# Performance work log

Hardware: AMD Instinct MI355X
Metric: run time of the kernel (lower is better)

The kernel has to match this reference:

```python
import jax, jax.numpy as jnp
import numpy as np

B, C, H, W, K = 64, 64, 32, 32, 512  # batch, embedding_dim, latent HxW, num_embeddings
COMMITMENT_COST = 0.25


def setup_inputs() -> dict:
    key = jax.random.key(0)
    k1, k2 = jax.random.split(key)
    inputs = jax.random.normal(k1, (B, C, H, W), dtype=jnp.float32)
    # nn.Embedding weight initialized uniform(-1/K, 1/K)
    weight = jax.random.uniform(k2, (K, C), minval=-1.0 / K, maxval=1.0 / K, dtype=jnp.float32)
    return {"inputs": inputs, "weight": weight}


def reference(inputs, weight):
    # NCHW -> NHWC
    x = jnp.transpose(inputs, (0, 2, 3, 1))  # [B,H,W,C]
    b, h, w, c = x.shape
    flat = x.reshape(-1, c)  # [N, C], N = B*H*W

    distances = (jnp.sum(flat * flat, axis=1, keepdims=True)
                 + jnp.sum(weight * weight, axis=1)[None, :]
                 - 2.0 * flat @ weight.T)

    idx = jnp.argmin(distances, axis=1)  # [N]
    encodings = jax.nn.one_hot(idx, weight.shape[0], dtype=flat.dtype)  # [N, K]

    # gather codebook vectors (same math as encodings @ weight)
    quantized = weight[idx].reshape(x.shape)  # [B,H,W,C]

    e_latent = jnp.mean((jax.lax.stop_gradient(quantized) - x) ** 2, axis=(1, 2, 3))
    q_latent = jnp.mean((quantized - jax.lax.stop_gradient(x)) ** 2, axis=(1, 2, 3))
    loss = q_latent + COMMITMENT_COST * e_latent  # [B]

    # straight-through estimator
    quantized_st = x + jax.lax.stop_gradient(quantized - x)

    avg_probs = jnp.mean(encodings, axis=0)  # [K]
    perplexity = jnp.exp(-jnp.sum(avg_probs * jnp.log(avg_probs + 1e-10)))

    q_out = jnp.transpose(quantized_st, (0, 3, 1, 2))  # back to NCHW
    enc_idx = idx.reshape(b, -1)  # [B, H*W]
    return (q_out, loss, perplexity, encodings, enc_idx, distances)
```

## Files before the change

### kernel.cpp

```cpp
#include <hip/hip_runtime.h>
#include <stdint.h>
#include <math.h>

#pragma clang fp contract(off)

#define B_   64
#define C_   64
#define HW_  1024
#define K_   512
#define N_   65536

#define OUT_Q    0ull
#define OUT_LOSS 4194304ull
#define OUT_PERP 4194368ull
#define OUT_ENC  4194369ull
#define OUT_IDX  37748801ull
#define OUT_DIST 37814337ull

#define WS_WT     0ull
#define WS_WNORM  131072ull
#define WS_HIST   133120ull
#define WS_SUMSQ  135168ull
#define WS_ZERO_BYTES (512*4 + 64*4)

typedef float f32x4 __attribute__((ext_vector_type(4)));

static __device__ __forceinline__ void nt_store4(float* p, float a, float b,
                                                 float c, float d) {
  f32x4 v = {a, b, c, d};
  __builtin_nontemporal_store(v, (f32x4*)p);
}

__global__ __launch_bounds__(256) void vq_prep(const float* __restrict__ w,
                                               float* __restrict__ wt,
                                               float* __restrict__ wnorm) {
  const int t = threadIdx.x;
  const int g = blockIdx.x * 256 + t;
  const int c = g >> 9;
  const int k = g & 511;
  wt[g] = w[k * 64 + c];

  if (blockIdx.x < 16) {
    const int row = g >> 3;
    const int j = g & 7;
    float s = 0.f;
    for (int i = 0; i < 8; ++i) {
      float v = w[row * 64 + 8 * i + j];
      float sq = v * v;
      s = s + sq;
    }
    float o1 = __shfl_xor(s, 1); s = s + o1;
    float o2 = __shfl_xor(s, 2); s = s + o2;
    float o4 = __shfl_xor(s, 4); s = s + o4;
    if (j == 0) wnorm[row] = s;
  }
}

__global__ __launch_bounds__(256, 4) void vq_main(const float* __restrict__ x,
                                                  const float* __restrict__ wt,
                                                  const float* __restrict__ wnorm,
                                                  float* __restrict__ out,
                                                  int* __restrict__ hist,
                                                  float* __restrict__ sumsq) {
  __shared__ float x_s[64 * 32];
  __shared__ float an_s[32];
  __shared__ int   kmin_s[32];
  __shared__ float red_s[4];

  const int t   = threadIdx.x;
  const int blk = blockIdx.x;
  const int n0  = blk * 32;
  const int b   = n0 >> 10;
  const int hw0 = n0 & 1023;
  const int wid = t >> 6;
  const int l   = t & 63;

  {
    const float* xb = x + (size_t)b * 65536 + hw0;
    const int c0 = t >> 3;
    const int m4 = (t & 7) * 4;
#pragma unroll
    for (int i = 0; i < 2; ++i) {
      int c = i * 32 + c0;
      float4 v = *(const float4*)(xb + (size_t)c * 1024 + m4);
      *(float4*)(&x_s[c * 32 + m4]) = v;
    }
  }
  __syncthreads();

  {
    const int r = t >> 3, j = t & 7;
    float s = 0.f;
#pragma unroll
    for (int i = 0; i < 8; ++i) {
      float v = x_s[(8 * i + j) * 32 + r];
      float sq = v * v;
      s = s + sq;
    }
    float o1 = __shfl_xor(s, 1); s = s + o1;
    float o2 = __shfl_xor(s, 2); s = s + o2;
    float o4 = __shfl_xor(s, 4); s = s + o4;
    if (j == 0) an_s[r] = s;
  }

  float wn[8];
  *(float4*)(wn)     = *(const float4*)(wnorm + 4 * l);
  *(float4*)(wn + 4) = *(const float4*)(wnorm + 256 + 4 * l);

  float acc[8][8];
#pragma unroll
  for (int i = 0; i < 8; ++i)
#pragma unroll
    for (int j = 0; j < 8; ++j) acc[i][j] = 0.f;

  const float* const wl = wt + 4 * l;
  const float* const xw = x_s + 8 * wid;
  float4 w0 = *(const float4*)(wl);
  float4 w1 = *(const float4*)(wl + 256);
#pragma unroll 2
  for (int c = 0; c < 64; ++c) {
    const int cn = (c + 1) & 63;
    const float4 nw0 = *(const float4*)(wl + cn * 512);
    const float4 nw1 = *(const float4*)(wl + cn * 512 + 256);
    float xv[8];
    *(float4*)(xv)     = *(const float4*)(xw + c * 32);
    *(float4*)(xv + 4) = *(const float4*)(xw + c * 32 + 4);
    const float wv0[4] = {w0.x, w0.y, w0.z, w0.w};
    const float wv1[4] = {w1.x, w1.y, w1.z, w1.w};
#pragma unroll
    for (int i = 0; i < 8; ++i) {
#pragma unroll
      for (int j = 0; j < 4; ++j) {
        acc[i][j]     = __builtin_fmaf(xv[i], wv0[j], acc[i][j]);
        acc[i][j + 4] = __builtin_fmaf(xv[i], wv1[j], acc[i][j + 4]);
      }
    }
    w0 = nw0; w1 = nw1;
  }

  const int m_base = 8 * wid;
  float vb[8]; int kb[8];
#pragma unroll
  for (int i = 0; i < 8; ++i) {
    const float an = an_s[m_base + i];
#pragma unroll
    for (int j = 0; j < 8; ++j) {
      float tt = an + wn[j];
      acc[i][j] = __builtin_fmaf(-2.f, acc[i][j], tt);
    }
    float v = acc[i][0]; int k = 4 * l;
#pragma unroll
    for (int j = 1; j < 8; ++j) {
      const int kj = ((j >> 2) << 8) + 4 * l + (j & 3);
      if (acc[i][j] < v) { v = acc[i][j]; k = kj; }
    }
    vb[i] = v; kb[i] = k;
  }

#pragma unroll
  for (int d = 1; d < 64; d <<= 1) {
#pragma unroll
    for (int i = 0; i < 8; ++i) {
      float v2 = __shfl_xor(vb[i], d);
      int   k2 = __shfl_xor(kb[i], d);
      if (v2 < vb[i] || (v2 == vb[i] && k2 < kb[i])) { vb[i] = v2; kb[i] = k2; }
    }
  }

  float* const dist_o = out + OUT_DIST;
  float* const enc_o  = out + OUT_ENC;
#pragma unroll
  for (int i = 0; i < 8; ++i) {
    const int m = m_base + i;
    const size_t n = (size_t)(n0 + m);
    float* dr = dist_o + n * 512;
    float* er = enc_o  + n * 512;
    nt_store4(dr + 4 * l,       acc[i][0], acc[i][1], acc[i][2], acc[i][3]);
    nt_store4(dr + 256 + 4 * l, acc[i][4], acc[i][5], acc[i][6], acc[i][7]);
    const int kbi = kb[i];
    const int k0 = 4 * l;
    nt_store4(er + 4 * l,
              (k0 + 0 == kbi) ? 1.f : 0.f, (k0 + 1 == kbi) ? 1.f : 0.f,
              (k0 + 2 == kbi) ? 1.f : 0.f, (k0 + 3 == kbi) ? 1.f : 0.f);
    nt_store4(er + 256 + 4 * l,
              (k0 + 256 == kbi) ? 1.f : 0.f, (k0 + 257 == kbi) ? 1.f : 0.f,
              (k0 + 258 == kbi) ? 1.f : 0.f, (k0 + 259 == kbi) ? 1.f : 0.f);
    if (l == i) {
      out[OUT_IDX + n] = (float)kbi;
      atomicAdd(&hist[kbi], 1);
      kmin_s[m] = kbi;
    }
  }
  __syncthreads();

  float lsum = 0.f;
  float* const q_o = out + OUT_Q;
#pragma unroll
  for (int it = 0; it < 2; ++it) {
    const int c  = it * 32 + (t >> 3);
    const int m4 = (t & 7) * 4;
    float xq[4];
    *(float4*)(xq) = *(const float4*)(&x_s[c * 32 + m4]);
    float qv[4];
#pragma unroll
    for (int u = 0; u < 4; ++u) {
      const int kbm = kmin_s[m4 + u];
      qv[u] = wt[(size_t)c * 512 + kbm];
      const float d = qv[u] - xq[u];
      lsum = __builtin_fmaf(d, d, lsum);
    }
    nt_store4(&q_o[(size_t)b * 65536 + (size_t)c * 1024 + hw0 + m4],
              qv[0], qv[1], qv[2], qv[3]);
  }
#pragma unroll
  for (int d = 1; d < 64; d <<= 1) lsum += __shfl_xor(lsum, d);
  if (l == 0) red_s[wid] = lsum;
  __syncthreads();
  if (t == 0) {
    float s = (red_s[0] + red_s[1]) + (red_s[2] + red_s[3]);
    atomicAdd(sumsq + b, s);
  }
}

__global__ __launch_bounds__(512) void vq_fin(const int* __restrict__ hist,
                                              const float* __restrict__ sumsq,
                                              float* __restrict__ out) {
  __shared__ double red[8];
  const int t = threadIdx.x;
  double p = (double)hist[t] * (1.0 / 65536.0);
  double term = p * log(p + 1e-10);
  for (int d = 1; d < 64; d <<= 1) term += __shfl_xor(term, d);
  if ((t & 63) == 0) red[t >> 6] = term;
  __syncthreads();
  if (t == 0) {
    double s = 0.0;
    for (int i = 0; i < 8; ++i) s += red[i];
    out[OUT_PERP] = (float)exp(-s);
  }
  if (t < 64) {
    float m = sumsq[t] * (1.0f / 65536.0f);
    out[OUT_LOSS + t] = m + 0.25f * m;
  }
}

extern "C" void kernel_launch(void* const* d_in, const int* in_sizes, int n_in,
                              void* d_out, int out_size, void* d_ws, size_t ws_size,
                              hipStream_t stream) {
  const float* x = (const float*)d_in[0];
  const float* w = (const float*)d_in[1];
  float* out = (float*)d_out;
  char* ws = (char*)d_ws;
  float* wt    = (float*)(ws + WS_WT);
  float* wnorm = (float*)(ws + WS_WNORM);
  int*   hist  = (int*)  (ws + WS_HIST);
  float* sumsq = (float*)(ws + WS_SUMSQ);

  (void)hipMemsetAsync(ws + WS_HIST, 0, WS_ZERO_BYTES, stream);
  vq_prep<<<128, 256, 0, stream>>>(w, wt, wnorm);
  vq_main<<<2048, 256, 0, stream>>>(x, wt, wnorm, out, hist, sumsq);
  vq_fin<<<1, 512, 0, stream>>>(hist, sumsq, out);
}
```

Before: 354.6 us.

## Split main kernel into distance/argmin kernel and encoding/quantize kernel

Splits the fused main kernel in two. The first kernel computes distances, argmin, the index output and the histogram. The second reads the indices back from the output buffer and writes the one-hot encodings, quantized values and loss partial sums, re-reading x from global memory. This removes register and LDS pressure and the trailing barriers from the compute kernel and lets the store-heavy part run at higher occupancy, at the cost of an extra launch and re-reading x and the indices.

After: 358.9 us. About the same (+1.2%).

```diff
diff --git a/kernel.cpp b/kernel.cpp
--- a/kernel.cpp
+++ b/kernel.cpp
@@ -56,16 +56,13 @@
   }
 }
 
-__global__ __launch_bounds__(256, 4) void vq_main(const float* __restrict__ x,
+__global__ __launch_bounds__(256, 4) void vq_dist(const float* __restrict__ x,
                                                   const float* __restrict__ wt,
                                                   const float* __restrict__ wnorm,
                                                   float* __restrict__ out,
-                                                  int* __restrict__ hist,
-                                                  float* __restrict__ sumsq) {
+                                                  int* __restrict__ hist) {
   __shared__ float x_s[64 * 32];
   __shared__ float an_s[32];
-  __shared__ int   kmin_s[32];
-  __shared__ float red_s[4];
 
   const int t   = threadIdx.x;
   const int blk = blockIdx.x;
@@ -168,30 +165,50 @@
   }
 
   float* const dist_o = out + OUT_DIST;
-  float* const enc_o  = out + OUT_ENC;
 #pragma unroll
   for (int i = 0; i < 8; ++i) {
     const int m = m_base + i;
     const size_t n = (size_t)(n0 + m);
     float* dr = dist_o + n * 512;
-    float* er = enc_o  + n * 512;
     nt_store4(dr + 4 * l,       acc[i][0], acc[i][1], acc[i][2], acc[i][3]);
     nt_store4(dr + 256 + 4 * l, acc[i][4], acc[i][5], acc[i][6], acc[i][7]);
-    const int kbi = kb[i];
-    const int k0 = 4 * l;
-    nt_store4(er + 4 * l,
+    if (l == i) {
+      out[OUT_IDX + n] = (float)kb[i];
+      atomicAdd(&hist[kb[i]], 1);
+    }
+  }
+}
+
+__global__ __launch_bounds__(256, 8) void vq_q(const float* __restrict__ x,
+                                               const float* __restrict__ wt,
+                                               float* __restrict__ out,
+                                               float* __restrict__ sumsq) {
+  __shared__ float red_s[4];
+
+  const int t   = threadIdx.x;
+  const int blk = blockIdx.x;
+  const int n0  = blk * 32;
+  const int b   = n0 >> 10;
+  const int hw0 = n0 & 1023;
+  const int wid = t >> 6;
+  const int l   = t & 63;
+
+  const float* const idx_f = out + OUT_IDX + n0;
+
+  float* const enc_o = out + OUT_ENC;
+  const int k0 = 4 * l;
+#pragma unroll
+  for (int i = 0; i < 8; ++i) {
+    const int m = 8 * wid + i;
+    const int kbi = (int)idx_f[m];
+    float* er = enc_o + (size_t)(n0 + m) * 512;
+    nt_store4(er + k0,
               (k0 + 0 == kbi) ? 1.f : 0.f, (k0 + 1 == kbi) ? 1.f : 0.f,
               (k0 + 2 == kbi) ? 1.f : 0.f, (k0 + 3 == kbi) ? 1.f : 0.f);
-    nt_store4(er + 256 + 4 * l,
+    nt_store4(er + 256 + k0,
               (k0 + 256 == kbi) ? 1.f : 0.f, (k0 + 257 == kbi) ? 1.f : 0.f,
               (k0 + 258 == kbi) ? 1.f : 0.f, (k0 + 259 == kbi) ? 1.f : 0.f);
-    if (l == i) {
-      out[OUT_IDX + n] = (float)kbi;
-      atomicAdd(&hist[kbi], 1);
-      kmin_s[m] = kbi;
-    }
-  }
-  __syncthreads();
+  }
 
   float lsum = 0.f;
   float* const q_o = out + OUT_Q;
@@ -200,11 +217,12 @@
     const int c  = it * 32 + (t >> 3);
     const int m4 = (t & 7) * 4;
     float xq[4];
-    *(float4*)(xq) = *(const float4*)(&x_s[c * 32 + m4]);
+    *(float4*)(xq) = *(const float4*)(x + (size_t)b * 65536 +
+                                      (size_t)c * 1024 + hw0 + m4);
     float qv[4];
 #pragma unroll
     for (int u = 0; u < 4; ++u) {
-      const int kbm = kmin_s[m4 + u];
+      const int kbm = (int)idx_f[m4 + u];
       qv[u] = wt[(size_t)c * 512 + kbm];
       const float d = qv[u] - xq[u];
       lsum = __builtin_fmaf(d, d, lsum);
@@ -257,6 +275,7 @@
 
   (void)hipMemsetAsync(ws + WS_HIST, 0, WS_ZERO_BYTES, stream);
   vq_prep<<<128, 256, 0, stream>>>(w, wt, wnorm);
-  vq_main<<<2048, 256, 0, stream>>>(x, wt, wnorm, out, hist, sumsq);
+  vq_dist<<<2048, 256, 0, stream>>>(x, wt, wnorm, out, hist);
+  vq_q<<<2048, 256, 0, stream>>>(x, wt, out, sumsq);
   vq_fin<<<1, 512, 0, stream>>>(hist, sumsq, out);
 }
```
